# Kernel optimization log

Measured on AMD Instinct MI355X. Metric: run time of the kernel, lower is better.

The kernel has to match this reference:

```python
import jax, jax.numpy as jnp
import numpy as np
from jax import lax

B, CIN, COUT, K = 256, 3, 16, 3
D, H, W_ = 16, 32, 32
POOL = 4


def setup_inputs() -> dict:
    key = jax.random.key(0)
    kx, kw, kb = jax.random.split(key, 3)
    x = jax.random.normal(kx, (B, CIN, D, H, W_), dtype=jnp.float32)
    # Conv3d default init scale ~ 1/sqrt(fan_in)
    fan_in = CIN * K * K * K
    bound = 1.0 / np.sqrt(fan_in)
    W = jax.random.uniform(kw, (COUT, CIN, K, K, K), dtype=jnp.float32, minval=-bound, maxval=bound)
    b = jax.random.uniform(kb, (COUT,), dtype=jnp.float32, minval=-bound, maxval=bound)
    return {"x": x, "W": W, "b": b}


def reference(x, W, b):
    # Conv3d, valid padding, stride 1: [B,16,14,30,30]
    y = lax.conv_general_dilated(
        x, W, window_strides=(1, 1, 1), padding="VALID",
        dimension_numbers=("NCDHW", "OIDHW", "NCDHW"))
    y = y + b[None, :, None, None, None]
    # channel softmax (dim=1)
    s = jax.nn.softmax(y, axis=1)
    # 4x4x4 max-pool, stride 4, no padding: [B,16,3,7,7]
    out = lax.reduce_window(
        s, -jnp.inf, lax.max,
        window_dimensions=(1, 1, POOL, POOL, POOL),
        window_strides=(1, 1, POOL, POOL, POOL),
        padding="VALID")
    return out
```

## Files before the change

kernel.cpp:

```cpp
#include <hip/hip_runtime.h>
#include <math.h>

#define BATCH 256
#define CIN   3
#define COUT  16
#define DI    16
#define HI    32
#define WI    32

typedef _Float16 f16;
typedef f16   f16x4 __attribute__((ext_vector_type(4)));
typedef f16   f16x8 __attribute__((ext_vector_type(8)));
typedef float f32x4 __attribute__((ext_vector_type(4)));

#define LOG2E 1.44269504088896340736f

#define ROWU   144
#define PLANEU 4320
#define XS_N   (6 * PLANEU)
#define G8OFF  (2 * PLANEU + 2 * ROWU)

#define SV8(a, b) __builtin_shufflevector(a, b, 0, 1, 2, 3, 4, 5, 6, 7)
#define MFMA16(A, B, C) __builtin_amdgcn_mfma_f32_16x16x32_f16(A, B, C, 0, 0, 0)

#define DPPMAX(v, ctrl) do {                                                  \
    int t_ = __builtin_amdgcn_update_dpp(                                     \
        0, __builtin_bit_cast(int, v), (ctrl), 0xF, 0xF, false);              \
    v = fmaxf(v, __builtin_bit_cast(float, t_));                              \
} while (0)

__global__ __launch_bounds__(512, 6) void conv_sm_pool_mfma(
    const float* __restrict__ x, const float* __restrict__ W,
    const float* __restrict__ bias, float* __restrict__ out)
{
    __shared__ __align__(16) f16 xs[XS_N];

    const int tid  = threadIdx.x;
    const int lane = tid & 63;
    const int wave = tid >> 6;
    const int b    = blockIdx.x / 3;
    const int pd   = blockIdx.x % 3;
    const int d0   = pd * 4;

    const int col = lane & 15;
    const int kq  = lane >> 4;

    const float* wc  = W + col * 81;
    const float* wqp = wc + kq * 6;
    f16x8 wm[3];
    #pragma unroll
    for (int kw = 0; kw < 3; ++kw) {
        #pragma unroll
        for (int j = 0; j < 8; ++j) {
            const int ci = j & 3, jj = j >> 2;
            float v = (ci < 3) ? wqp[ci * 27 + 3 * jj + kw] * LOG2E : 0.f;
            wm[kw][j] = (f16)v;
        }
    }
    f16x8 wg = {};
    if (kq == 0) {
        #pragma unroll
        for (int j = 0; j < 8; ++j) {
            const int ci = j & 3, kw = j >> 2;
            if (ci < 3) wg[j] = (f16)(wc[ci * 27 + 24 + kw] * LOG2E);
        }
    } else if (kq == 1) {
        #pragma unroll
        for (int j = 0; j < 3; ++j) wg[j] = (f16)(wc[j * 27 + 26] * LOG2E);
    }
    const float4 braw = *(const float4*)(bias + kq * 4);
    float4 bv;
    bv.x = braw.x * LOG2E; bv.y = braw.y * LOG2E;
    bv.z = braw.z * LOG2E; bv.w = braw.w * LOG2E;

    for (int i = tid; i < 1440; i += 512) {
        int wqd = i & 7;
        int r   = i >> 3;
        int hh  = r % 30;
        int dd  = r / 30;
        const float* px = x + ((size_t)b * 48 + (d0 + dd)) * 1024 + hh * 32 + wqd * 4;
        float4 a0 = *(const float4*)(px);
        float4 a1 = *(const float4*)(px + 16384);
        float4 a2 = *(const float4*)(px + 32768);
        f16x8 p0, p1;
        p0[0] = (f16)a0.x; p0[1] = (f16)a1.x; p0[2] = (f16)a2.x; p0[3] = (f16)0.f;
        p0[4] = (f16)a0.y; p0[5] = (f16)a1.y; p0[6] = (f16)a2.y; p0[7] = (f16)0.f;
        p1[0] = (f16)a0.z; p1[1] = (f16)a1.z; p1[2] = (f16)a2.z; p1[3] = (f16)0.f;
        p1[4] = (f16)a0.w; p1[5] = (f16)a1.w; p1[6] = (f16)a2.w; p1[7] = (f16)0.f;
        f16* dst = xs + ((dd * 30 + hh) * 36 + wqd * 4) * 4;
        *(f16x8*)(dst)     = p0;
        *(f16x8*)(dst + 8) = p1;
    }

    const int g0   = kq * 2;
    const int off1 = (g0 / 3) * PLANEU + (g0 % 3) * ROWU;
    const int off2 = ((g0 + 1) / 3) * PLANEU + ((g0 + 1) % 3) * ROWU;
    const int hl = col >> 2, wl = col & 3;
    const int spat  = hl * ROWU + wl * 4;
    const int g8sel = (kq == 0) ? 0 : 8;

    __syncthreads();

    for (int c = wave; c < 49; c += 8) {
        const int ch = c / 7;
        const int pw = c - ch * 7;
        const f16* base = xs + ch * 4 * ROWU + pw * 16 + spat;
        const f16* a1 = base + off1;
        const f16* a2 = base + off2;
        const f16* a3 = base + G8OFF + g8sel;

        f16x4 Bv[4][8];
        #pragma unroll
        for (int d = 0; d < 4; ++d) {
            const int dp = d * PLANEU;
            Bv[d][0] = *(const f16x4*)(a1 + dp);
            Bv[d][1] = *(const f16x4*)(a2 + dp);
            Bv[d][2] = *(const f16x4*)(a1 + dp + 4);
            Bv[d][3] = *(const f16x4*)(a2 + dp + 4);
            Bv[d][4] = *(const f16x4*)(a1 + dp + 8);
            Bv[d][5] = *(const f16x4*)(a2 + dp + 8);
            Bv[d][6] = *(const f16x4*)(a3 + dp);
            Bv[d][7] = *(const f16x4*)(a3 + dp + 4);
        }

        f32x4 acc[4];
        #pragma unroll
        for (int d = 0; d < 4; ++d) {
            f32x4 a_ = {0.f, 0.f, 0.f, 0.f};
            a_ = MFMA16(wm[0], SV8(Bv[d][0], Bv[d][1]), a_);
            a_ = MFMA16(wm[1], SV8(Bv[d][2], Bv[d][3]), a_);
            a_ = MFMA16(wm[2], SV8(Bv[d][4], Bv[d][5]), a_);
            a_ = MFMA16(wg,    SV8(Bv[d][6], Bv[d][7]), a_);
            acc[d] = a_;
        }

        float ev[4][4], s[4];
        #pragma unroll
        for (int d = 0; d < 4; ++d) {
            float y0 = acc[d][0] + bv.x, y1 = acc[d][1] + bv.y;
            float y2 = acc[d][2] + bv.z, y3 = acc[d][3] + bv.w;
            ev[d][0] = __builtin_amdgcn_exp2f(y0);
            ev[d][1] = __builtin_amdgcn_exp2f(y1);
            ev[d][2] = __builtin_amdgcn_exp2f(y2);
            ev[d][3] = __builtin_amdgcn_exp2f(y3);
            s[d] = (ev[d][0] + ev[d][1]) + (ev[d][2] + ev[d][3]);
        }
        #pragma unroll
        for (int d = 0; d < 4; ++d) s[d] += __shfl_xor(s[d], 16);
        #pragma unroll
        for (int d = 0; d < 4; ++d) s[d] += __shfl_xor(s[d], 32);

        f32x4 pm = {0.f, 0.f, 0.f, 0.f};
        #pragma unroll
        for (int d = 0; d < 4; ++d) {
            float iv = __builtin_amdgcn_rcpf(s[d]);
            pm[0] = fmaxf(pm[0], ev[d][0] * iv);
            pm[1] = fmaxf(pm[1], ev[d][1] * iv);
            pm[2] = fmaxf(pm[2], ev[d][2] * iv);
            pm[3] = fmaxf(pm[3], ev[d][3] * iv);
        }

        #pragma unroll
        for (int r = 0; r < 4; ++r) {
            float v = pm[r];
            DPPMAX(v, 0x128);
            DPPMAX(v, 0x124);
            DPPMAX(v, 0x122);
            DPPMAX(v, 0x121);
            pm[r] = v;
        }

        if (col == 0) {
            float* po = out + ((size_t)b * COUT + kq * 4) * 147 + pd * 49 + c;
            po[0]   = pm[0];
            po[147] = pm[1];
            po[294] = pm[2];
            po[441] = pm[3];
        }
    }
}

extern "C" void kernel_launch(void* const* d_in, const int* in_sizes, int n_in,
                              void* d_out, int out_size, void* d_ws, size_t ws_size,
                              hipStream_t stream) {
    const float* x    = (const float*)d_in[0];
    const float* W    = (const float*)d_in[1];
    const float* bias = (const float*)d_in[2];
    float* out = (float*)d_out;

    conv_sm_pool_mfma<<<BATCH * 3, 512, 0, stream>>>(x, W, bias, out);
}
```

Baseline: 30.29 us.

## Fold bias into MFMA via ones channel and double-buffer LDS loads across depth slices

The padding channel in the shared-memory input tile is set to 1.0 instead of 0, and the bias is placed in the matching weight slot of the kq==0 lane group, so the MFMA adds the bias and the separate per-element bias adds go away. The per-depth loop is restructured into a ping-pong A/B register pipeline that issues the LDS loads for the next depth plane before computing the current one. This lowers register pressure compared with holding all 32 fragments and overlaps LDS latency with MFMA and exp work. The cost is that the bias is rounded to fp16, which slightly changes numerics.

New measurement: 29.78 us. No clear change (-1.7%).

```diff
diff --git a/kernel.cpp b/kernel.cpp
--- a/kernel.cpp
+++ b/kernel.cpp
@@ -27,6 +27,36 @@
     int t_ = __builtin_amdgcn_update_dpp(                                     \
         0, __builtin_bit_cast(int, v), (ctrl), 0xF, 0xF, false);              \
     v = fmaxf(v, __builtin_bit_cast(float, t_));                              \
+} while (0)
+
+#define LOADS(P, dp)                                                          \
+    P##0 = *(const f16x4*)(a1 + (dp));                                        \
+    P##1 = *(const f16x4*)(a2 + (dp));                                        \
+    P##2 = *(const f16x4*)(a1 + (dp) + 4);                                    \
+    P##3 = *(const f16x4*)(a2 + (dp) + 4);                                    \
+    P##4 = *(const f16x4*)(a1 + (dp) + 8);                                    \
+    P##5 = *(const f16x4*)(a2 + (dp) + 8);                                    \
+    P##6 = *(const f16x4*)(a3 + (dp));                                        \
+    P##7 = *(const f16x4*)(a3 + (dp) + 4);
+
+#define COMPUTE(P)  do {                                                      \
+    f32x4 a_ = {0.f, 0.f, 0.f, 0.f};                                          \
+    a_ = MFMA16(wm[0], SV8(P##0, P##1), a_);                                  \
+    a_ = MFMA16(wm[1], SV8(P##2, P##3), a_);                                  \
+    a_ = MFMA16(wm[2], SV8(P##4, P##5), a_);                                  \
+    a_ = MFMA16(wg,    SV8(P##6, P##7), a_);                                  \
+    float e0 = __builtin_amdgcn_exp2f(a_[0]);                                 \
+    float e1 = __builtin_amdgcn_exp2f(a_[1]);                                 \
+    float e2 = __builtin_amdgcn_exp2f(a_[2]);                                 \
+    float e3 = __builtin_amdgcn_exp2f(a_[3]);                                 \
+    float s_ = (e0 + e1) + (e2 + e3);                                         \
+    s_ += __shfl_xor(s_, 16);                                                 \
+    s_ += __shfl_xor(s_, 32);                                                 \
+    float iv = __builtin_amdgcn_rcpf(s_);                                     \
+    pm[0] = fmaxf(pm[0], e0 * iv);                                            \
+    pm[1] = fmaxf(pm[1], e1 * iv);                                            \
+    pm[2] = fmaxf(pm[2], e2 * iv);                                            \
+    pm[3] = fmaxf(pm[3], e3 * iv);                                            \
 } while (0)
 
 __global__ __launch_bounds__(512, 6) void conv_sm_pool_mfma(
@@ -64,14 +94,11 @@
             const int ci = j & 3, kw = j >> 2;
             if (ci < 3) wg[j] = (f16)(wc[ci * 27 + 24 + kw] * LOG2E);
         }
+        wg[3] = (f16)(bias[col] * LOG2E);
     } else if (kq == 1) {
         #pragma unroll
         for (int j = 0; j < 3; ++j) wg[j] = (f16)(wc[j * 27 + 26] * LOG2E);
     }
-    const float4 braw = *(const float4*)(bias + kq * 4);
-    float4 bv;
-    bv.x = braw.x * LOG2E; bv.y = braw.y * LOG2E;
-    bv.z = braw.z * LOG2E; bv.w = braw.w * LOG2E;
 
     for (int i = tid; i < 1440; i += 512) {
         int wqd = i & 7;
@@ -79,14 +106,14 @@
         int hh  = r % 30;
         int dd  = r / 30;
         const float* px = x + ((size_t)b * 48 + (d0 + dd)) * 1024 + hh * 32 + wqd * 4;
-        float4 a0 = *(const float4*)(px);
-        float4 a1 = *(const float4*)(px + 16384);
-        float4 a2 = *(const float4*)(px + 32768);
+        float4 v0 = *(const float4*)(px);
+        float4 v1 = *(const float4*)(px + 16384);
+        float4 v2 = *(const float4*)(px + 32768);
         f16x8 p0, p1;
-        p0[0] = (f16)a0.x; p0[1] = (f16)a1.x; p0[2] = (f16)a2.x; p0[3] = (f16)0.f;
-        p0[4] = (f16)a0.y; p0[5] = (f16)a1.y; p0[6] = (f16)a2.y; p0[7] = (f16)0.f;
-        p1[0] = (f16)a0.z; p1[1] = (f16)a1.z; p1[2] = (f16)a2.z; p1[3] = (f16)0.f;
-        p1[4] = (f16)a0.w; p1[5] = (f16)a1.w; p1[6] = (f16)a2.w; p1[7] = (f16)0.f;
+        p0[0] = (f16)v0.x; p0[1] = (f16)v1.x; p0[2] = (f16)v2.x; p0[3] = (f16)1.f;
+        p0[4] = (f16)v0.y; p0[5] = (f16)v1.y; p0[6] = (f16)v2.y; p0[7] = (f16)1.f;
+        p1[0] = (f16)v0.z; p1[1] = (f16)v1.z; p1[2] = (f16)v2.z; p1[3] = (f16)1.f;
+        p1[4] = (f16)v0.w; p1[5] = (f16)v1.w; p1[6] = (f16)v2.w; p1[7] = (f16)1.f;
         f16* dst = xs + ((dd * 30 + hh) * 36 + wqd * 4) * 4;
         *(f16x8*)(dst)     = p0;
         *(f16x8*)(dst + 8) = p1;
@@ -109,56 +136,18 @@
         const f16* a2 = base + off2;
         const f16* a3 = base + G8OFF + g8sel;
 
-        f16x4 Bv[4][8];
-        #pragma unroll
-        for (int d = 0; d < 4; ++d) {
-            const int dp = d * PLANEU;
-            Bv[d][0] = *(const f16x4*)(a1 + dp);
-            Bv[d][1] = *(const f16x4*)(a2 + dp);
-            Bv[d][2] = *(const f16x4*)(a1 + dp + 4);
-            Bv[d][3] = *(const f16x4*)(a2 + dp + 4);
-            Bv[d][4] = *(const f16x4*)(a1 + dp + 8);
-            Bv[d][5] = *(const f16x4*)(a2 + dp + 8);
-            Bv[d][6] = *(const f16x4*)(a3 + dp);
-            Bv[d][7] = *(const f16x4*)(a3 + dp + 4);
-        }
+        f32x4 pm = {0.f, 0.f, 0.f, 0.f};
 
-        f32x4 acc[4];
-        #pragma unroll
-        for (int d = 0; d < 4; ++d) {
-            f32x4 a_ = {0.f, 0.f, 0.f, 0.f};
-            a_ = MFMA16(wm[0], SV8(Bv[d][0], Bv[d][1]), a_);
-            a_ = MFMA16(wm[1], SV8(Bv[d][2], Bv[d][3]), a_);
-            a_ = MFMA16(wm[2], SV8(Bv[d][4], Bv[d][5]), a_);
-            a_ = MFMA16(wg,    SV8(Bv[d][6], Bv[d][7]), a_);
-            acc[d] = a_;
-        }
-
-        float ev[4][4], s[4];
-        #pragma unroll
-        for (int d = 0; d < 4; ++d) {
-            float y0 = acc[d][0] + bv.x, y1 = acc[d][1] + bv.y;
-            float y2 = acc[d][2] + bv.z, y3 = acc[d][3] + bv.w;
-            ev[d][0] = __builtin_amdgcn_exp2f(y0);
-            ev[d][1] = __builtin_amdgcn_exp2f(y1);
-            ev[d][2] = __builtin_amdgcn_exp2f(y2);
-            ev[d][3] = __builtin_amdgcn_exp2f(y3);
-            s[d] = (ev[d][0] + ev[d][1]) + (ev[d][2] + ev[d][3]);
-        }
-        #pragma unroll
-        for (int d = 0; d < 4; ++d) s[d] += __shfl_xor(s[d], 16);
-        #pragma unroll
-        for (int d = 0; d < 4; ++d) s[d] += __shfl_xor(s[d], 32);
-
-        f32x4 pm = {0.f, 0.f, 0.f, 0.f};
-        #pragma unroll
-        for (int d = 0; d < 4; ++d) {
-            float iv = __builtin_amdgcn_rcpf(s[d]);
-            pm[0] = fmaxf(pm[0], ev[d][0] * iv);
-            pm[1] = fmaxf(pm[1], ev[d][1] * iv);
-            pm[2] = fmaxf(pm[2], ev[d][2] * iv);
-            pm[3] = fmaxf(pm[3], ev[d][3] * iv);
-        }
+        f16x4 A0, A1, A2, A3, A4, A5, A6, A7;
+        f16x4 B0, B1, B2, B3, B4, B5, B6, B7;
+        LOADS(A, 0)
+        LOADS(B, PLANEU)
+        COMPUTE(A);
+        LOADS(A, 2 * PLANEU)
+        COMPUTE(B);
+        LOADS(B, 3 * PLANEU)
+        COMPUTE(A);
+        COMPUTE(B);
 
         #pragma unroll
         for (int r = 0; r < 4; ++r) {
```
